# Kernel optimization log

Hardware: AMD Instinct MI355X
Metric: run time of the kernel (lower is better)

Reference implementation:

```python
import jax, jax.numpy as jnp
import numpy as np

V, E, H, B, S = 32000, 1024, 1024, 64, 128


def setup_inputs() -> dict:
    key = jax.random.key(0)
    ks = jax.random.split(key, 16)
    s = 0.02
    return {
        "input_seq": jax.random.randint(ks[0], (B, 1), 0, V),
        "hidden": jax.random.normal(ks[1], (1, B, H), jnp.float32),
        "cell": jax.random.normal(ks[2], (1, B, H), jnp.float32),
        "encoder_outputs": jax.random.normal(ks[3], (B, S, H), jnp.float32),
        "emb": jax.random.normal(ks[4], (V, E), jnp.float32) * s,
        "Wa_w": jax.random.normal(ks[5], (H, H), jnp.float32) * s,
        "Wa_b": jnp.zeros((H,), jnp.float32),
        "Ua_w": jax.random.normal(ks[6], (H, H), jnp.float32) * s,
        "Ua_b": jnp.zeros((H,), jnp.float32),
        "Va_w": jax.random.normal(ks[7], (1, H), jnp.float32) * s,
        "Va_b": jnp.zeros((1,), jnp.float32),
        "W_ih": jax.random.normal(ks[8], (4 * H, E + H), jnp.float32) * s,
        "W_hh": jax.random.normal(ks[9], (4 * H, H), jnp.float32) * s,
        "b_ih": jnp.zeros((4 * H,), jnp.float32),
        "b_hh": jnp.zeros((4 * H,), jnp.float32),
        "out_w": jax.random.normal(ks[10], (V, H), jnp.float32) * s,
        "out_b": jnp.zeros((V,), jnp.float32),
    }


def reference(input_seq, hidden, cell, encoder_outputs, emb, Wa_w, Wa_b, Ua_w, Ua_b,
              Va_w, Va_b, W_ih, W_hh, b_ih, b_hh, out_w, out_b):
    # embedding lookup (dropout p=0 -> identity): [B,1,E]
    embedded = emb[input_seq]
    # query = last layer hidden: [B,1,H]
    query = hidden[-1][:, None, :]
    # Bahdanau additive attention
    q_proj = query @ Wa_w.T + Wa_b                       # [B,1,H]
    k_proj = encoder_outputs @ Ua_w.T + Ua_b             # [B,S,H]
    scores = jnp.tanh(q_proj + k_proj) @ Va_w.T + Va_b   # [B,S,1]
    scores = scores[..., 0][:, None, :]                  # [B,1,S]
    weights = jax.nn.softmax(scores, axis=-1)            # [B,1,S]
    context = jnp.einsum('bqs,bsh->bqh', weights, encoder_outputs)  # [B,1,H]
    # LSTM single step on concat(embedded, context)
    x = jnp.concatenate([embedded, context], axis=2)[:, 0, :]  # [B,E+H]
    h0, c0 = hidden[0], cell[0]
    gates = x @ W_ih.T + b_ih + h0 @ W_hh.T + b_hh       # [B,4H]
    i, f, g, o = jnp.split(gates, 4, axis=-1)
    c1 = jax.nn.sigmoid(f) * c0 + jax.nn.sigmoid(i) * jnp.tanh(g)
    h1 = jax.nn.sigmoid(o) * jnp.tanh(c1)
    output = h1[:, None, :]                              # [B,1,H]
    logits = output @ out_w.T + out_b                    # [B,1,V]
    return logits, h1[None], c1[None], weights
```

## Files before the change

### kernel.cpp

```cpp
#include <hip/hip_runtime.h>
#include <hip/hip_bf16.h>

using short8 = __attribute__((ext_vector_type(8))) short;
using f32x4  = __attribute__((ext_vector_type(4))) float;

__device__ inline unsigned pk2(float lo, float hi) {
    __hip_bfloat162 h = __float22bfloat162_rn(float2{lo, hi});
    return *reinterpret_cast<unsigned*>(&h);
}
__device__ inline short8 cvt8(float4 a, float4 b) {
    union { unsigned u[4]; short8 s; } r;
    r.u[0] = pk2(a.x, a.y); r.u[1] = pk2(a.z, a.w);
    r.u[2] = pk2(b.x, b.y); r.u[3] = pk2(b.z, b.w);
    return r.s;
}
__device__ inline float ftanh(float x) {
    float e = __expf(2.f * x);
    return 1.f - 2.f / (e + 1.f);
}
__device__ inline void gload16(const void* g, void* lds) {
    __builtin_amdgcn_global_load_lds(
        (const __attribute__((address_space(1))) unsigned int*)g,
        (__attribute__((address_space(3))) unsigned int*)lds, 16, 0, 0);
}

__global__ void k_init(const float* __restrict__ ob, float* __restrict__ logits,
                       const int* __restrict__ idx, const float* __restrict__ emb,
                       const float* __restrict__ h0, float* __restrict__ xcat,
                       float4* __restrict__ wsz) {
    int i = blockIdx.x * blockDim.x + threadIdx.x;
    if (i < 83968) {
        float4 z = {0.f, 0.f, 0.f, 0.f};
        wsz[i] = z;
    } else if (i < 595968) {
        int j = i - 83968;
        int c4 = j - (j / 8000) * 8000;
        ((float4*)logits)[j] = ((const float4*)ob)[c4];
    } else if (i < 645120) {
        int j = i - 595968;
        int b = j / 768, q = j - b * 768;
        if (q < 256)
            ((float4*)(xcat + (size_t)b * 3072))[q] =
                ((const float4*)(emb + (size_t)idx[b] * 1024))[q];
        else if (q >= 512)
            ((float4*)(xcat + (size_t)b * 3072))[q] =
                ((const float4*)(h0 + (size_t)b * 1024))[q - 512];
    }
}

__global__ void k_cvt_swz(const float* __restrict__ enc, const float* __restrict__ Ua,
                          short* __restrict__ dst) {
    int i = blockIdx.x * blockDim.x + threadIdx.x;
    if (i >= 9216 * 128) return;
    int row = i >> 7, gi = i & 127;
    int seg = gi >> 3, g = gi & 7;
    const float* src = (row < 8192) ? enc + ((size_t)row << 10)
                                    : Ua + ((size_t)(row - 8192) << 10);
    const float* p = src + (seg << 6) + ((g ^ (row & 7)) << 3);
    float4 v0 = *(const float4*)p;
    float4 v1 = *(const float4*)(p + 4);
    *(short8*)&dst[(size_t)i << 3] = cvt8(v0, v1);
}

__global__ __launch_bounds__(512) void k_attn2(
    const short* __restrict__ Abf, const short* __restrict__ Bbf,
    const float* __restrict__ Uab, const float* __restrict__ Wab,
    const float* __restrict__ qp, const float* __restrict__ Va,
    float* __restrict__ scores) {
    __shared__ short As[256 * 64];
    __shared__ short Bs[128 * 64];
    const int t = threadIdx.x;
    const int l = t & 63, w = t >> 6;
    const int wm = w >> 1, wn = w & 1;
    const int lr = l & 15, lg = l >> 4;
    const int n0 = blockIdx.x * 128;
    const int r0 = blockIdx.y * 256;

    f32x4 acc[4][4];
#pragma unroll
    for (int i = 0; i < 4; ++i)
#pragma unroll
        for (int j = 0; j < 4; ++j) { f32x4 z = {0.f, 0.f, 0.f, 0.f}; acc[i][j] = z; }

    for (int seg = 0; seg < 16; ++seg) {
#pragma unroll
        for (int i = 0; i < 4; ++i) {
            int base = i * 512 + w * 64;
            int s = base + l;
            gload16(Abf + (((size_t)r0 + (s >> 3)) << 10) + (seg << 6) + ((s & 7) << 3),
                    (void*)&As[base * 8]);
            if (i < 2)
                gload16(Bbf + (((size_t)8192 + n0 + (s >> 3)) << 10) + (seg << 6) + ((s & 7) << 3),
                        (void*)&Bs[base * 8]);
        }
        __syncthreads();
#pragma unroll
        for (int kh = 0; kh < 2; ++kh) {
            short8 a[4], b[4];
#pragma unroll
            for (int i = 0; i < 4; ++i) {
                int ra = wm * 64 + i * 16 + lr;
                a[i] = *(const short8*)&As[ra * 64 + (((kh * 4 + lg) ^ (ra & 7)) << 3)];
                int rb = wn * 64 + i * 16 + lr;
                b[i] = *(const short8*)&Bs[rb * 64 + (((kh * 4 + lg) ^ (rb & 7)) << 3)];
            }
#pragma unroll
            for (int i = 0; i < 4; ++i)
#pragma unroll
                for (int j = 0; j < 4; ++j)
                    acc[i][j] = __builtin_amdgcn_mfma_f32_16x16x32_bf16(a[i], b[j], acc[i][j], 0, 0, 0);
        }
        __syncthreads();
    }

    float va[4], ub[4];
#pragma unroll
    for (int j = 0; j < 4; ++j) {
        int h = n0 + wn * 64 + j * 16 + lr;
        va[j] = Va[h];
        ub[j] = Uab[h] + Wab[h];
    }
#pragma unroll
    for (int i = 0; i < 4; ++i)
#pragma unroll
        for (int r = 0; r < 4; ++r) {
            int row = r0 + wm * 64 + i * 16 + lg * 4 + r;
            const float* qpb = qp + (size_t)(row >> 7) * 1024;
            float s = 0.f;
#pragma unroll
            for (int j = 0; j < 4; ++j) {
                int h = n0 + wn * 64 + j * 16 + lr;
                s += va[j] * ftanh(acc[i][j][r] + qpb[h] + ub[j]);
            }
            s += __shfl_xor(s, 1);
            s += __shfl_xor(s, 2);
            s += __shfl_xor(s, 4);
            s += __shfl_xor(s, 8);
            if (lr == 0) atomicAdd(scores + row, s);
        }
}

__global__ __launch_bounds__(256) void k_sgemm(
    const float* __restrict__ A, int lda,
    const float* __restrict__ B0, int ldb0,
    const float* __restrict__ B1, int ldb1, int kyB1,
    float* __restrict__ C, int ldc, int Kblk) {
    __shared__ short As[64 * 64];
    __shared__ short Bs[64 * 64];
    const int t = threadIdx.x;
    const int l = t & 63, w = t >> 6;
    const int wm = w >> 1, wn = w & 1;
    const int lr = l & 15, lg = l >> 4;
    const int n0 = blockIdx.x * 64;
    const int ky = blockIdx.y;

    const float* Ab = A + (size_t)ky * Kblk;
    const float* Bb;
    int ldb;
    if (ky < kyB1) { Bb = B0 + (size_t)ky * Kblk; ldb = ldb0; }
    else           { Bb = B1 + (size_t)(ky - kyB1) * Kblk; ldb = ldb1; }

    f32x4 acc[2][2];
#pragma unroll
    for (int i = 0; i < 2; ++i)
#pragma unroll
        for (int j = 0; j < 2; ++j) { f32x4 z = {0.f, 0.f, 0.f, 0.f}; acc[i][j] = z; }

    for (int kt = 0; kt < Kblk; kt += 64) {
#pragma unroll
        for (int i = 0; i < 2; ++i) {
            int s = t + 256 * i, row = s >> 3, ch = s & 7;
            const float* p = Ab + (size_t)row * lda + kt + ch * 8;
            *(short8*)&As[row * 64 + ((ch ^ (row & 7)) << 3)] =
                cvt8(*(const float4*)p, *(const float4*)(p + 4));
            const float* q = Bb + (size_t)(n0 + row) * ldb + kt + ch * 8;
            *(short8*)&Bs[row * 64 + ((ch ^ (row & 7)) << 3)] =
                cvt8(*(const float4*)q, *(const float4*)(q + 4));
        }
        __syncthreads();
#pragma unroll
        for (int kh = 0; kh < 2; ++kh) {
            short8 a[2], b[2];
#pragma unroll
            for (int i = 0; i < 2; ++i) {
                int ra = wm * 32 + i * 16 + lr;
                a[i] = *(const short8*)&As[ra * 64 + (((kh * 4 + lg) ^ (ra & 7)) << 3)];
                int rb = wn * 32 + i * 16 + lr;
                b[i] = *(const short8*)&Bs[rb * 64 + (((kh * 4 + lg) ^ (rb & 7)) << 3)];
            }
#pragma unroll
            for (int i = 0; i < 2; ++i)
#pragma unroll
                for (int j = 0; j < 2; ++j)
                    acc[i][j] = __builtin_amdgcn_mfma_f32_16x16x32_bf16(a[i], b[j], acc[i][j], 0, 0, 0);
        }
        __syncthreads();
    }

#pragma unroll
    for (int i = 0; i < 2; ++i)
#pragma unroll
        for (int j = 0; j < 2; ++j)
#pragma unroll
            for (int r = 0; r < 4; ++r) {
                int R = wm * 32 + i * 16 + lg * 4 + r;
                int c = n0 + wn * 32 + j * 16 + lr;
                atomicAdd(&C[(size_t)R * ldc + c], acc[i][j][r]);
            }
}

__global__ __launch_bounds__(256) void k_smctx(
    const float* __restrict__ scores, const float* __restrict__ enc,
    float* __restrict__ wout, float* __restrict__ xcat) {
    int b = blockIdx.x;
    int t = threadIdx.x;
    __shared__ float buf[128];
    __shared__ float wsb[128];
    if (t < 128) buf[t] = scores[b * 128 + t];
    __syncthreads();
    if (t < 64) buf[t] = fmaxf(buf[t], buf[t + 64]);
    __syncthreads();
    if (t < 32) buf[t] = fmaxf(buf[t], buf[t + 32]);
    __syncthreads();
    float m;
    {
        float v = buf[t & 31];
        for (int off = 16; off > 0; off >>= 1)
            v = fmaxf(v, __shfl_xor(v, off, 32));
        m = v;
    }
    __syncthreads();
    if (t < 128) wsb[t] = __expf(scores[b * 128 + t] - m);
    __syncthreads();
    if (t < 64) buf[t] = wsb[t] + wsb[t + 64];
    __syncthreads();
    if (t < 32) buf[t] += buf[t + 32];
    __syncthreads();
    float sum;
    {
        float v = buf[t & 31];
        for (int off = 16; off > 0; off >>= 1)
            v += __shfl_xor(v, off, 32);
        sum = v;
    }
    float inv = 1.f / sum;
    __syncthreads();
    if (t < 128) {
        wsb[t] *= inv;
        wout[b * 128 + t] = wsb[t];
    }
    __syncthreads();
    float acc[4] = {0.f, 0.f, 0.f, 0.f};
    for (int s = 0; s < 128; ++s) {
        float wv = wsb[s];
        const float* row = enc + ((size_t)b * 128 + s) * 1024;
#pragma unroll
        for (int j = 0; j < 4; ++j) acc[j] += wv * row[t + 256 * j];
    }
#pragma unroll
    for (int j = 0; j < 4; ++j) xcat[(size_t)b * 3072 + 1024 + t + 256 * j] = acc[j];
}

__global__ void k_lstm(const float* __restrict__ gates, const float* __restrict__ c0,
                       const float* __restrict__ b_ih, const float* __restrict__ b_hh,
                       float* __restrict__ h1, float* __restrict__ c1) {
    int idx = blockIdx.x * blockDim.x + threadIdx.x;
    int b = idx >> 10, h = idx & 1023;
    const float* g = gates + (size_t)b * 4096;
    float iv = g[h] + b_ih[h] + b_hh[h];
    float fv = g[1024 + h] + b_ih[1024 + h] + b_hh[1024 + h];
    float gv = g[2048 + h] + b_ih[2048 + h] + b_hh[2048 + h];
    float ov = g[3072 + h] + b_ih[3072 + h] + b_hh[3072 + h];
    float si = 1.f / (1.f + expf(-iv));
    float sf = 1.f / (1.f + expf(-fv));
    float so = 1.f / (1.f + expf(-ov));
    float tg = tanhf(gv);
    float cc = sf * c0[idx] + si * tg;
    float hh = so * tanhf(cc);
    c1[idx] = cc;
    h1[idx] = hh;
}

extern "C" void kernel_launch(void* const* d_in, const int* in_sizes, int n_in,
                              void* d_out, int out_size, void* d_ws, size_t ws_size,
                              hipStream_t stream) {
    const int* idx = (const int*)d_in[0];
    const float* hidden = (const float*)d_in[1];
    const float* cell = (const float*)d_in[2];
    const float* enc = (const float*)d_in[3];
    const float* emb = (const float*)d_in[4];
    const float* Wa_w = (const float*)d_in[5];
    const float* Wa_b = (const float*)d_in[6];
    const float* Ua_w = (const float*)d_in[7];
    const float* Ua_b = (const float*)d_in[8];
    const float* Va_w = (const float*)d_in[9];
    const float* W_ih = (const float*)d_in[11];
    const float* W_hh = (const float*)d_in[12];
    const float* b_ih = (const float*)d_in[13];
    const float* b_hh = (const float*)d_in[14];
    const float* out_w = (const float*)d_in[15];
    const float* out_b = (const float*)d_in[16];

    float* out = (float*)d_out;
    float* logits = out;
    float* h1 = out + 2048000;
    float* c1 = out + 2048000 + 65536;
    float* wts = out + 2048000 + 65536 + 65536;

    float* ws = (float*)d_ws;
    float* qp = ws;
    float* scores = ws + 65536;
    float* gates = ws + 73728;
    float* xcat = ws + 335872;
    short* encua_bf = (short*)(ws + 532480);

    k_init<<<2520, 256, 0, stream>>>(out_b, logits, idx, emb, hidden, xcat,
                                     (float4*)ws);
    k_cvt_swz<<<4608, 256, 0, stream>>>(enc, Ua_w, encua_bf);
    k_sgemm<<<dim3(16, 8), 256, 0, stream>>>(hidden, 1024, Wa_w, 1024,
                                             nullptr, 0, 99, qp, 1024, 128);
    k_attn2<<<dim3(8, 32), 512, 0, stream>>>(encua_bf, encua_bf, Ua_b, Wa_b,
                                             qp, Va_w, scores);
    k_smctx<<<64, 256, 0, stream>>>(scores, enc, wts, xcat);
    k_sgemm<<<dim3(64, 12), 256, 0, stream>>>(xcat, 3072, W_ih, 2048,
                                              W_hh, 1024, 8, gates, 4096, 256);
    k_lstm<<<256, 256, 0, stream>>>(gates, cell, b_ih, b_hh, h1, c1);
    k_sgemm<<<dim3(500, 4), 256, 0, stream>>>(h1, 1024, out_w, 1024,
                                              nullptr, 0, 99, logits, 32000, 256);
}
```

Baseline: 135.0 us.

## Replace split-K atomic accumulation with partial buffers and separate reduction passes

The gates and logits split-K GEMMs now write each K-slice's partial result to its own workspace buffer with plain stores instead of atomicAdd onto a pre-initialised output. The LSTM kernel sums the six gate partials (split-K reduced from 12 to 6 slices), and a new reduction kernel sums four logits partials and adds the output bias. This removes the atomic traffic and the bias/zero-initialisation of logits in k_init, at the cost of an extra kernel launch and writing and re-reading roughly 32 MB of logits partials.

```diff
diff --git a/kernel.cpp b/kernel.cpp
--- a/kernel.cpp
+++ b/kernel.cpp
@@ -24,20 +24,15 @@
         (__attribute__((address_space(3))) unsigned int*)lds, 16, 0, 0);
 }
 
-__global__ void k_init(const float* __restrict__ ob, float* __restrict__ logits,
-                       const int* __restrict__ idx, const float* __restrict__ emb,
+__global__ void k_init(const int* __restrict__ idx, const float* __restrict__ emb,
                        const float* __restrict__ h0, float* __restrict__ xcat,
                        float4* __restrict__ wsz) {
     int i = blockIdx.x * blockDim.x + threadIdx.x;
-    if (i < 83968) {
+    if (i < 18432) {
         float4 z = {0.f, 0.f, 0.f, 0.f};
         wsz[i] = z;
-    } else if (i < 595968) {
-        int j = i - 83968;
-        int c4 = j - (j / 8000) * 8000;
-        ((float4*)logits)[j] = ((const float4*)ob)[c4];
-    } else if (i < 645120) {
-        int j = i - 595968;
+    } else if (i < 67584) {
+        int j = i - 18432;
         int b = j / 768, q = j - b * 768;
         if (q < 256)
             ((float4*)(xcat + (size_t)b * 3072))[q] =
@@ -140,11 +135,12 @@
         }
 }
 
+template <int EPI>
 __global__ __launch_bounds__(256) void k_sgemm(
     const float* __restrict__ A, int lda,
     const float* __restrict__ B0, int ldb0,
     const float* __restrict__ B1, int ldb1, int kyB1,
-    float* __restrict__ C, int ldc, int Kblk) {
+    float* __restrict__ C, int ldc, int Kblk, int pstride) {
     __shared__ short As[64 * 64];
     __shared__ short Bs[64 * 64];
     const int t = threadIdx.x;
@@ -197,6 +193,7 @@
         __syncthreads();
     }
 
+    float* Cp = (EPI == 0) ? C + (size_t)ky * pstride : C;
 #pragma unroll
     for (int i = 0; i < 2; ++i)
 #pragma unroll
@@ -205,7 +202,10 @@
             for (int r = 0; r < 4; ++r) {
                 int R = wm * 32 + i * 16 + lg * 4 + r;
                 int c = n0 + wn * 32 + j * 16 + lr;
-                atomicAdd(&C[(size_t)R * ldc + c], acc[i][j][r]);
+                if constexpr (EPI == 1)
+                    atomicAdd(&C[(size_t)R * ldc + c], acc[i][j][r]);
+                else
+                    Cp[(size_t)R * ldc + c] = acc[i][j][r];
             }
 }
 
@@ -261,16 +261,24 @@
     for (int j = 0; j < 4; ++j) xcat[(size_t)b * 3072 + 1024 + t + 256 * j] = acc[j];
 }
 
-__global__ void k_lstm(const float* __restrict__ gates, const float* __restrict__ c0,
-                       const float* __restrict__ b_ih, const float* __restrict__ b_hh,
-                       float* __restrict__ h1, float* __restrict__ c1) {
+__global__ void k_lstm6(const float* __restrict__ gp, const float* __restrict__ c0,
+                        const float* __restrict__ b_ih, const float* __restrict__ b_hh,
+                        float* __restrict__ h1, float* __restrict__ c1) {
     int idx = blockIdx.x * blockDim.x + threadIdx.x;
     int b = idx >> 10, h = idx & 1023;
-    const float* g = gates + (size_t)b * 4096;
-    float iv = g[h] + b_ih[h] + b_hh[h];
-    float fv = g[1024 + h] + b_ih[1024 + h] + b_hh[1024 + h];
-    float gv = g[2048 + h] + b_ih[2048 + h] + b_hh[2048 + h];
-    float ov = g[3072 + h] + b_ih[3072 + h] + b_hh[3072 + h];
+    const float* g0 = gp + (size_t)b * 4096;
+    float iv = b_ih[h] + b_hh[h];
+    float fv = b_ih[1024 + h] + b_hh[1024 + h];
+    float gv = b_ih[2048 + h] + b_hh[2048 + h];
+    float ov = b_ih[3072 + h] + b_hh[3072 + h];
+#pragma unroll
+    for (int p = 0; p < 6; ++p) {
+        const float* g = g0 + p * 262144;
+        iv += g[h];
+        fv += g[1024 + h];
+        gv += g[2048 + h];
+        ov += g[3072 + h];
+    }
     float si = 1.f / (1.f + expf(-iv));
     float sf = 1.f / (1.f + expf(-fv));
     float so = 1.f / (1.f + expf(-ov));
@@ -279,6 +287,20 @@
     float hh = so * tanhf(cc);
     c1[idx] = cc;
     h1[idx] = hh;
+}
+
+__global__ void k_red4(const float* __restrict__ lp, const float* __restrict__ ob,
+                       float* __restrict__ logits) {
+    int i = blockIdx.x * blockDim.x + threadIdx.x;
+    if (i >= 512000) return;
+    int c4 = i - (i / 8000) * 8000;
+    float4 s = ((const float4*)ob)[c4];
+#pragma unroll
+    for (int p = 0; p < 4; ++p) {
+        float4 v = ((const float4*)(lp + (size_t)p * 2048000))[i];
+        s.x += v.x; s.y += v.y; s.z += v.z; s.w += v.w;
+    }
+    ((float4*)logits)[i] = s;
 }
 
 extern "C" void kernel_launch(void* const* d_in, const int* in_sizes, int n_in,
@@ -310,21 +332,22 @@
     float* ws = (float*)d_ws;
     float* qp = ws;
     float* scores = ws + 65536;
-    float* gates = ws + 73728;
-    float* xcat = ws + 335872;
-    short* encua_bf = (short*)(ws + 532480);
-
-    k_init<<<2520, 256, 0, stream>>>(out_b, logits, idx, emb, hidden, xcat,
-                                     (float4*)ws);
+    float* xcat = ws + 73728;
+    float* gates_p = ws + 270336;
+    float* logits_p = ws + 1843200;
+    short* encua_bf = (short*)(ws + 10035200);
+
+    k_init<<<264, 256, 0, stream>>>(idx, emb, hidden, xcat, (float4*)ws);
     k_cvt_swz<<<4608, 256, 0, stream>>>(enc, Ua_w, encua_bf);
-    k_sgemm<<<dim3(16, 8), 256, 0, stream>>>(hidden, 1024, Wa_w, 1024,
-                                             nullptr, 0, 99, qp, 1024, 128);
+    k_sgemm<1><<<dim3(16, 8), 256, 0, stream>>>(hidden, 1024, Wa_w, 1024,
+                                                nullptr, 0, 99, qp, 1024, 128, 0);
     k_attn2<<<dim3(8, 32), 512, 0, stream>>>(encua_bf, encua_bf, Ua_b, Wa_b,
                                              qp, Va_w, scores);
     k_smctx<<<64, 256, 0, stream>>>(scores, enc, wts, xcat);
-    k_sgemm<<<dim3(64, 12), 256, 0, stream>>>(xcat, 3072, W_ih, 2048,
-                                              W_hh, 1024, 8, gates, 4096, 256);
-    k_lstm<<<256, 256, 0, stream>>>(gates, cell, b_ih, b_hh, h1, c1);
-    k_sgemm<<<dim3(500, 4), 256, 0, stream>>>(h1, 1024, out_w, 1024,
-                                              nullptr, 0, 99, logits, 32000, 256);
-}
+    k_sgemm<0><<<dim3(64, 6), 256, 0, stream>>>(xcat, 3072, W_ih, 2048,
+                                                W_hh, 1024, 4, gates_p, 4096, 512, 262144);
+    k_lstm6<<<256, 256, 0, stream>>>(gates_p, cell, b_ih, b_hh, h1, c1);
+    k_sgemm<0><<<dim3(500, 4), 256, 0, stream>>>(h1, 1024, out_w, 1024,
+                                                 nullptr, 0, 99, logits_p, 32000, 256, 2048000);
+    k_red4<<<2000, 256, 0, stream>>>(logits_p, out_b, logits);
+}
```

Measured after the change: 138.3 us. 1.02x slower.
